# Kernel optimization log

Measured on AMD Instinct MI355X. Metric: run time of the kernel, lower is better.

Reference implementation:

```python
import jax, jax.numpy as jnp
import numpy as np

B, N, C = 4, 4096, 128
IK, CK = 9, 9  # inner_k, cross_k
BN_EPS = 1e-5


def setup_inputs() -> dict:
    key = jax.random.key(0)
    ks = jax.random.split(key, 8)
    d = {}
    d["x"] = jax.random.normal(ks[0], (B, N, C), jnp.float32)
    d["y"] = jax.random.normal(ks[1], (B, N, C), jnp.float32)
    d["x_mask"] = jnp.ones((B, N), jnp.float32)
    d["y_mask"] = jnp.ones((B, N), jnp.float32)
    specs = [("mr0", C, 2 * C), ("mr1", C, 2 * C), ("fc", C, C), ("f1", 4 * C, C), ("f2", C, 4 * C)]
    for (name, o, i), k in zip(specs, jax.random.split(ks[2], len(specs))):
        d[name + "_W"] = jax.random.normal(k, (o, i), jnp.float32) * 0.05
        d[name + "_b"] = jnp.zeros((o,), jnp.float32)
        d[name + "_g"] = jnp.ones((o,), jnp.float32)
        d[name + "_beta"] = jnp.zeros((o,), jnp.float32)
        d[name + "_m"] = jnp.zeros((o,), jnp.float32)
        d[name + "_v"] = jnp.ones((o,), jnp.float32)
    return d


def _sqdist(a, b):
    # a: [B,Na,C], b: [B,Nb,C] -> [B,Na,Nb]
    return (jnp.sum(a * a, -1)[:, :, None] + jnp.sum(b * b, -1)[:, None, :]
            - 2.0 * jnp.einsum('bnc,bmc->bnm', a, b))


def _knn(x, y):
    # neighbor indices into concat([x;y]) for every node: [B, Nx+Ny, IK+CK]
    Nx = x.shape[1]
    i_xx = jax.lax.top_k(-_sqdist(x, x), IK)[1]
    i_xy = jax.lax.top_k(-_sqdist(x, y), CK)[1] + Nx
    i_yy = jax.lax.top_k(-_sqdist(y, y), IK)[1] + Nx
    i_yx = jax.lax.top_k(-_sqdist(y, x), CK)[1]
    return jnp.concatenate([jnp.concatenate([i_xx, i_xy], -1),
                            jnp.concatenate([i_yy, i_yx], -1)], axis=1)


def _bn(h, g, b, m, v):
    # eval-mode BatchNorm over channel (last) axis
    return (h - m) * jax.lax.rsqrt(v + BN_EPS) * g + b


def _gelu(h):
    return jax.nn.gelu(h, approximate=False)


def _mrconv(f, nbr, W, b, g, be, m, v):
    # f: [B,Nt,C], nbr: [B,Nt,K] -> Conv(2C->C)+BN+GELU of interleaved [x, max_j(x_j-x_i)]
    xj = jax.vmap(lambda fb, nb: fb[nb])(f, nbr)          # [B,Nt,K,C] gather
    msg = jnp.max(xj - f[:, :, None, :], axis=2)          # [B,Nt,C]
    Bh, Nt, Ch = f.shape
    h = jnp.stack([f, msg], axis=-1).reshape(Bh, Nt, 2 * Ch)  # channel interleave as in torch reshape
    h = jnp.einsum('bnc,oc->bno', h, W) + b
    return _gelu(_bn(h, g, be, m, v))


def _forward(x, x_mask, y, y_mask,
             mr0_W, mr0_b, mr0_g, mr0_beta, mr0_m, mr0_v,
             mr1_W, mr1_b, mr1_g, mr1_beta, mr1_m, mr1_v,
             fc_W, fc_b, fc_g, fc_beta, fc_m, fc_v,
             f1_W, f1_b, f1_g, f1_beta, f1_m, f1_v,
             f2_W, f2_b, f2_g, f2_beta, f2_m, f2_v):
    Nx = x.shape[1]
    nbr = _knn(x, y)
    xy = jnp.concatenate([x, y], axis=1)
    xy = _mrconv(xy, nbr, mr0_W, mr0_b, mr0_g, mr0_beta, mr0_m, mr0_v) + xy
    xy = _mrconv(xy, nbr, mr1_W, mr1_b, mr1_g, mr1_beta, mr1_m, mr1_v) + xy
    xg, yg = xy[:, :Nx], xy[:, Nx:]

    def fc(h):
        return _bn(jnp.einsum('bnc,oc->bno', h, fc_W) + fc_b, fc_g, fc_beta, fc_m, fc_v)

    xo = fc(xg) + x
    yo = fc(yg) + y

    def ffn(h):
        r = h
        h = _gelu(_bn(jnp.einsum('bnc,oc->bno', h, f1_W) + f1_b, f1_g, f1_beta, f1_m, f1_v))
        h = _gelu(_bn(jnp.einsum('bnc,oc->bno', h, f2_W) + f2_b, f2_g, f2_beta, f2_m, f2_v))
        return h + r

    xo = ffn(xo) * x_mask[:, :, None]
    yo = ffn(yo) * y_mask[:, :, None]
    return xo, yo


def reference(x, x_mask, y, y_mask,
              mr0_W, mr0_b, mr0_g, mr0_beta, mr0_m, mr0_v,
              mr1_W, mr1_b, mr1_g, mr1_beta, mr1_m, mr1_v,
              fc_W, fc_b, fc_g, fc_beta, fc_m, fc_v,
              f1_W, f1_b, f1_g, f1_beta, f1_m, f1_v,
              f2_W, f2_b, f2_g, f2_beta, f2_m, f2_v):
    return _forward(x, x_mask, y, y_mask,
                    mr0_W, mr0_b, mr0_g, mr0_beta, mr0_m, mr0_v,
                    mr1_W, mr1_b, mr1_g, mr1_beta, mr1_m, mr1_v,
                    fc_W, fc_b, fc_g, fc_beta, fc_m, fc_v,
                    f1_W, f1_b, f1_g, f1_beta, f1_m, f1_v,
                    f2_W, f2_b, f2_g, f2_beta, f2_m, f2_v)
```

## Files before the change

### kernel.cpp

```cpp
#include <hip/hip_runtime.h>
#include <hip/hip_bf16.h>
#include <float.h>
#include <math.h>

#define BB 4
#define N1 4096
#define NT 8192
#define CH 128
#define NBRS 18
#define ZSEL 2.35f
#define LCAP 40
#define EQ 4096.0f
#define GQGAP 6
#define GQCOV 3

typedef __attribute__((ext_vector_type(8))) short s16x8;
typedef __attribute__((ext_vector_type(16))) float f32x16;
typedef __attribute__((ext_vector_type(4))) float f32x4;

__device__ inline unsigned short f2bf(float v) {
  unsigned u = __float_as_uint(v);
  unsigned r = (u + 0x7FFFu + ((u >> 16) & 1u)) >> 16;
  return (unsigned short)r;
}
__device__ inline float bf2f(unsigned short h) {
  return __uint_as_float((unsigned)h << 16);
}
__device__ inline unsigned mapf(float f) {
  unsigned u = __float_as_uint(f);
  return (u & 0x80000000u) ? ~u : (u | 0x80000000u);
}
__device__ inline float gelu_f(float x) {
  return 0.5f * x * (1.0f + erff(x * 0.70710678118654752f));
}

__global__ __launch_bounds__(256) void transpose_k(const float* __restrict__ in,
                                                   float* __restrict__ out,
                                                   int rows, int cols) {
  int t = blockIdx.x * 256 + threadIdx.x;
  if (t < rows * cols) {
    int r = t / cols, c = t % cols;
    out[c * rows + r] = in[t];
  }
}

__global__ __launch_bounds__(256) void wsplit_k(const float* __restrict__ w,
                                                unsigned short* __restrict__ hi,
                                                unsigned short* __restrict__ lo,
                                                int n) {
  int t = blockIdx.x * 256 + threadIdx.x;
  if (t < n) {
    float v = w[t];
    unsigned short h = f2bf(v);
    float r = v - bf2f(h);
    hi[t] = h; lo[t] = f2bf(r);
  }
}

__global__ __launch_bounds__(256) void norms_concat_k(const float* __restrict__ x,
                                                      const float* __restrict__ y,
                                                      float* __restrict__ xy,
                                                      float* __restrict__ norms) {
  int w = (blockIdx.x * 256 + threadIdx.x) >> 6;
  int lane = threadIdx.x & 63;
  int b = w >> 13, row = w & 8191;
  const float* src = (row < N1) ? (x + ((size_t)b * N1 + row) * CH)
                                : (y + ((size_t)b * N1 + (row - N1)) * CH);
  float2 v = *(const float2*)(src + lane * 2);
  *(float2*)(xy + (size_t)w * CH + lane * 2) = v;
  float s = v.x * v.x + v.y * v.y;
  for (int off = 32; off > 0; off >>= 1) s += __shfl_down(s, off);
  if (lane == 0) norms[w] = s;
}

__global__ __launch_bounds__(256) void cbt_k(const float* __restrict__ xy,
                                             unsigned short* __restrict__ cbt) {
  int t = blockIdx.x * 256 + threadIdx.x;
  int u = t >> 15, p = t & 32767;
  const float* src = xy + (size_t)p * CH + u * 8;
  unsigned hw[4], lw[4];
#pragma unroll
  for (int j = 0; j < 4; ++j) {
    float v0 = src[2 * j], v1 = src[2 * j + 1];
    unsigned short h0 = f2bf(v0), h1 = f2bf(v1);
    float r0 = v0 - bf2f(h0);
    float r1 = v1 - bf2f(h1);
    unsigned short l0 = f2bf(r0), l1 = f2bf(r1);
    hw[j] = (unsigned)h0 | ((unsigned)h1 << 16);
    lw[j] = (unsigned)l0 | ((unsigned)l1 << 16);
  }
  *(uint4*)&cbt[((size_t)u * 32768 + p) * 8] = make_uint4(hw[0], hw[1], hw[2], hw[3]);
  *(uint4*)&cbt[((size_t)(u + 16) * 32768 + p) * 8] = make_uint4(lw[0], lw[1], lw[2], lw[3]);
}

__global__ __launch_bounds__(256) void knn4_k(const unsigned short* __restrict__ cbt,
                                              const float* __restrict__ norms,
                                              int* __restrict__ nbr,
                                              int* __restrict__ cntg,
                                              unsigned* __restrict__ listA,
                                              unsigned* __restrict__ listB,
                                              unsigned short* __restrict__ fbl) {
  __shared__ unsigned short __align__(16) cst[2][32][32][8];
  __shared__ float cn_s[2][32];
  __shared__ unsigned lst[128][2][LCAP];
  __shared__ unsigned short lcnt[128][2];
  const int tid = threadIdx.x;
  const int qblk = blockIdx.x, z = blockIdx.y;
  const int b = z >> 2, combo = z & 3;
  const int qoff = (combo <= 1) ? 0 : N1;
  const int coff = (combo == 0 || combo == 3) ? 0 : N1;
  const int w = tid >> 6;
  const int cl = tid & 31;
  const int h = (tid >> 5) & 1;
  const int h4 = 4 * h;
  const int ql = w * 32 + cl;
  const int q = qblk * 128 + ql;
  const size_t qp = (size_t)b * NT + qoff + q;
  const size_t cb0 = (size_t)b * NT + coff;

  const s16x8* cv = (const s16x8*)cbt;
  s16x8 bh[8], bl[8];
#pragma unroll
  for (int s = 0; s < 8; ++s) {
    bh[s] = cv[(size_t)(2 * s + h) * 32768 + qp];
    bl[s] = cv[(size_t)(16 + 2 * s + h) * 32768 + qp];
  }

  const float nq = norms[qp];
  const float Tc = 128.f - ZSEL * sqrtf(256.f + 4.f * nq);
  int cnt = 0;

  const int su = tid >> 5, sc = tid & 31;
  const char* p0 = (const char*)&cbt[((size_t)(su) * 32768 + cb0 + sc) * 8];
  const char* p1 = (const char*)&cbt[((size_t)(8 + su) * 32768 + cb0 + sc) * 8];
  const char* p2 = (const char*)&cbt[((size_t)(16 + su) * 32768 + cb0 + sc) * 8];
  const char* p3 = (const char*)&cbt[((size_t)(24 + su) * 32768 + cb0 + sc) * 8];
  const float* pn = norms + cb0 + tid;

  uint4 st[4]; float cnreg = 0.f;
  st[0] = *(const uint4*)p0; p0 += 512;
  st[1] = *(const uint4*)p1; p1 += 512;
  st[2] = *(const uint4*)p2; p2 += 512;
  st[3] = *(const uint4*)p3; p3 += 512;
  if (tid < 32) { cnreg = *pn; pn += 32; }
  *(uint4*)&cst[0][su][sc][0] = st[0];
  *(uint4*)&cst[0][8 + su][sc][0] = st[1];
  *(uint4*)&cst[0][16 + su][sc][0] = st[2];
  *(uint4*)&cst[0][24 + su][sc][0] = st[3];
  if (tid < 32) cn_s[0][tid] = cnreg;
  __syncthreads();

  int buf = 0;
  for (int t = 0; t < 128; ++t) {
    if (t < 127) {
      st[0] = *(const uint4*)p0; p0 += 512;
      st[1] = *(const uint4*)p1; p1 += 512;
      st[2] = *(const uint4*)p2; p2 += 512;
      st[3] = *(const uint4*)p3; p3 += 512;
      if (tid < 32) { cnreg = *pn; pn += 32; }
    }
    f32x16 acc = {0.f,0.f,0.f,0.f,0.f,0.f,0.f,0.f,0.f,0.f,0.f,0.f,0.f,0.f,0.f,0.f};
#pragma unroll
    for (int s = 0; s < 8; ++s) {
      s16x8 a0 = *(const s16x8*)&cst[buf][2 * s + h][cl][0];
      s16x8 a1 = *(const s16x8*)&cst[buf][16 + 2 * s + h][cl][0];
      acc = __builtin_amdgcn_mfma_f32_32x32x16_bf16(a0, bh[s], acc, 0, 0, 0);
      acc = __builtin_amdgcn_mfma_f32_32x32x16_bf16(a0, bl[s], acc, 0, 0, 0);
      acc = __builtin_amdgcn_mfma_f32_32x32x16_bf16(a1, bh[s], acc, 0, 0, 0);
    }
    float4 c0 = *(const float4*)&cn_s[buf][h4];
    float4 c1 = *(const float4*)&cn_s[buf][8 + h4];
    float4 c2 = *(const float4*)&cn_s[buf][16 + h4];
    float4 c3 = *(const float4*)&cn_s[buf][24 + h4];
    const float cw[16] = {c0.x, c0.y, c0.z, c0.w, c1.x, c1.y, c1.z, c1.w,
                          c2.x, c2.y, c2.z, c2.w, c3.x, c3.y, c3.z, c3.w};
    const int ib = t * 32 + h4;
#pragma unroll
    for (int g = 0; g < 4; ++g) {
#pragma unroll
      for (int rr = 0; rr < 4; ++rr) {
        const int r = g * 4 + rr;
        float s = fmaf(-2.0f, acc[r], cw[r]);
        if (s <= Tc) {
          int e = (int)((Tc - s) * EQ);
          e = e > 0xFFFFF ? 0xFFFFF : e;
          unsigned key = ((unsigned)e << 12) | (unsigned)(4095 - (ib + g * 8 + rr));
          if (cnt < LCAP) lst[ql][h][cnt] = key;
          ++cnt;
        }
      }
    }
    if (t < 127) {
      *(uint4*)&cst[buf ^ 1][su][sc][0] = st[0];
      *(uint4*)&cst[buf ^ 1][8 + su][sc][0] = st[1];
      *(uint4*)&cst[buf ^ 1][16 + su][sc][0] = st[2];
      *(uint4*)&cst[buf ^ 1][24 + su][sc][0] = st[3];
      if (tid < 32) cn_s[buf ^ 1][tid] = cnreg;
    }
    __syncthreads();
    buf ^= 1;
  }
  lcnt[ql][h] = (unsigned short)cnt;
  __syncthreads();

  if (tid < 128) {
    const int mq = tid;
    const int gq = z * 4096 + qblk * 128 + mq;
    const int c0 = lcnt[mq][0], c1 = lcnt[mq][1];
    const bool over = (c0 > LCAP) || (c1 > LCAP);
    const int n0 = c0 > LCAP ? LCAP : c0;
    const int n1 = c1 > LCAP ? LCAP : c1;
    const int m = n0 + n1;
    unsigned top[10];
#pragma unroll
    for (int j = 0; j < 10; ++j) top[j] = 0u;
    for (int li = 0; li < 2; ++li) {
      const int n = li ? n1 : n0;
      for (int i = 0; i < n; ++i) {
        unsigned key = lst[mq][li][i];
        if (key > top[9]) {
#pragma unroll
          for (int j = 0; j < 10; ++j) {
            bool sw = key > top[j];
            unsigned tv = top[j];
            top[j] = sw ? key : tv;
            key = sw ? tv : key;
          }
        }
      }
    }
    const unsigned e8 = top[8] >> 12, e9 = top[9] >> 12;
    const bool cov = !over && (m >= 9) && (e8 >= GQCOV);
    const bool ok = cov && (m == 9 || (e8 - e9) >= GQGAP);
    const int qg = qblk * 128 + mq;
    const int row = (combo <= 1) ? qg : (N1 + qg);
    const int slot = (combo == 0 || combo == 2) ? 0 : 9;
    const int ioff = (combo == 1 || combo == 2) ? N1 : 0;
    int* dst = nbr + ((size_t)b * NT + row) * NBRS + slot;
    if (ok) {
#pragma unroll
      for (int s = 0; s < 9; ++s)
        dst[s] = (int)(4095u - (top[s] & 0xFFFu)) + ioff;
    } else if (!cov || m > 64) {
      int idx = atomicAdd(&cntg[1], 1);
      listB[idx] = (unsigned)gq;
    } else {
      int idx = atomicAdd(&cntg[0], 1);
      listA[idx] = ((unsigned)m << 16) | (unsigned)gq;
      unsigned short* fp = fbl + (size_t)gq * 64;
      int p = 0;
      for (int i = 0; i < n0; ++i) fp[p++] = (unsigned short)(4095u - (lst[mq][0][i] & 0xFFFu));
      for (int i = 0; i < n1; ++i) fp[p++] = (unsigned short)(4095u - (lst[mq][1][i] & 0xFFFu));
    }
  }
}

__global__ __launch_bounds__(256) void rerank_sl_k(const float* __restrict__ xy,
                                                   const float* __restrict__ norms,
                                                   const unsigned short* __restrict__ fbl,
                                                   const unsigned* __restrict__ listA,
                                                   const int* __restrict__ cntg,
                                                   int* __restrict__ nbr) {
  const int lane = threadIdx.x & 63;
  const int wv = threadIdx.x >> 6;
  const int nA = cntg[0];
  for (int i = blockIdx.x * 4 + wv; i < nA; i += gridDim.x * 4) {
    const unsigned ent = listA[i];
    const int gq = (int)(ent & 0xffffu);
    const int m = (int)(ent >> 16);
    const int z = gq >> 12, q = gq & 4095;
    const int b = z >> 2, combo = z & 3;
    const int qoff = (combo <= 1) ? 0 : N1;
    const int coff = (combo == 0 || combo == 3) ? 0 : N1;
    const size_t cq = (size_t)b * NT + coff;
    const int row = (combo <= 1) ? q : (N1 + q);
    const int slot = (combo == 0 || combo == 2) ? 0 : 9;
    const int ioff = (combo == 1 || combo == 2) ? N1 : 0;
    int* dst = nbr + ((size_t)b * NT + row) * NBRS + slot;
    const float* qrow = xy + ((size_t)b * NT + qoff + q) * CH;

    int ci = 0; float de = FLT_MAX;
    if (lane < m) {
      ci = (int)fbl[(size_t)gq * 64 + lane];
      const float* crow = xy + (cq + ci) * CH;
      const float cnv = norms[cq + ci];
      float a0 = 0.f, a1 = 0.f, a2 = 0.f, a3 = 0.f;
#pragma unroll
      for (int k = 0; k < 32; ++k) {
        float4 qv = *(const float4*)(qrow + k * 4);
        float4 cv2 = *(const float4*)(crow + k * 4);
        a0 = fmaf(qv.x, cv2.x, a0); a1 = fmaf(qv.y, cv2.y, a1);
        a2 = fmaf(qv.z, cv2.z, a2); a3 = fmaf(qv.w, cv2.w, a3);
      }
      de = cnv - 2.0f * ((a0 + a1) + (a2 + a3));
    }
    unsigned long long key = ((unsigned long long)mapf(de) << 32) | (unsigned)ci;
    if (lane >= m) key = ~0ull;
    int xr = 0;
#pragma unroll 1
    for (int k = 0; k < m; ++k) {
      unsigned long long kk = __shfl(key, k);
      xr += (kk < key) ? 1 : 0;
    }
    if (lane < m && xr < 9) dst[xr] = ci + ioff;
  }
}

__global__ __launch_bounds__(256) void rerank_fs_k(const float* __restrict__ xy,
                                                   const float* __restrict__ norms,
                                                   const unsigned* __restrict__ listB,
                                                   const int* __restrict__ cntg,
                                                   int* __restrict__ nbr) {
  __shared__ unsigned long long ms[4][576];
  __shared__ unsigned long long wk[36];
  const int tid = threadIdx.x;
  const int lane = tid & 63, wv = tid >> 6;
  const int nB = cntg[1];
  for (int i = blockIdx.x; i < nB; i += gridDim.x) {
    const int gq = (int)listB[i];
    const int z = gq >> 12, q = gq & 4095;
    const int b = z >> 2, combo = z & 3;
    const int qoff = (combo <= 1) ? 0 : N1;
    const int coff = (combo == 0 || combo == 3) ? 0 : N1;
    const size_t cq = (size_t)b * NT + coff;
    const int row = (combo <= 1) ? q : (N1 + q);
    const int slot = (combo == 0 || combo == 2) ? 0 : 9;
    const int ioff = (combo == 1 || combo == 2) ? N1 : 0;
    int* dst = nbr + ((size_t)b * NT + row) * NBRS + slot;
    const float* qrow = xy + ((size_t)b * NT + qoff + q) * CH;

    unsigned long long bl9[9];
#pragma unroll
    for (int j = 0; j < 9; ++j) bl9[j] = ~0ull;
    for (int it = 0; it < 16; ++it) {
      const int cc = (it * 4 + wv) * 64 + lane;
      const float* crow = xy + (cq + cc) * CH;
      float a0 = 0.f, a1 = 0.f, a2 = 0.f, a3 = 0.f;
#pragma unroll
      for (int k = 0; k < 32; ++k) {
        float4 qv = *(const float4*)(qrow + k * 4);
        float4 cv2 = *(const float4*)(crow + k * 4);
        a0 = fmaf(qv.x, cv2.x, a0); a1 = fmaf(qv.y, cv2.y, a1);
        a2 = fmaf(qv.z, cv2.z, a2); a3 = fmaf(qv.w, cv2.w, a3);
      }
      float d2v = norms[cq + cc] - 2.0f * ((a0 + a1) + (a2 + a3));
      unsigned long long key = ((unsigned long long)mapf(d2v) << 32) | (unsigned)cc;
      if (key < bl9[8]) {
#pragma unroll
        for (int jj = 0; jj < 9; ++jj) {
          bool sw = key < bl9[jj];
          unsigned long long tv = bl9[jj];
          bl9[jj] = sw ? key : tv;
          key = sw ? tv : key;
        }
      }
    }
#pragma unroll
    for (int s = 0; s < 9; ++s) ms[wv][lane * 9 + s] = bl9[s];
    int ptr = 0;
    for (int s = 0; s < 9; ++s) {
      unsigned long long hd = ms[wv][lane * 9 + ptr];
      unsigned long long mn = hd;
#pragma unroll
      for (int off = 1; off < 64; off <<= 1) {
        unsigned long long ot = __shfl_xor(mn, off);
        mn = (ot < mn) ? ot : mn;
      }
      unsigned long long wm = __ballot(hd == mn);
      int wl = __ffsll(wm) - 1;
      if (lane == wl) ptr++;
      if (lane == 0) wk[wv * 9 + s] = mn;
    }
    __syncthreads();
    if (wv == 0) {
      unsigned long long key = (lane < 36) ? wk[lane] : ~0ull;
      int xr = 0;
#pragma unroll 1
      for (int k = 0; k < 36; ++k) {
        unsigned long long kk = __shfl(key, k);
        xr += (kk < key) ? 1 : 0;
      }
      if (lane < 36 && xr < 9) dst[xr] = (int)(unsigned)(key & 0xffffffffull) + ioff;
    }
    __syncthreads();
  }
}

__global__ __launch_bounds__(256) void mrconv_k(const float* __restrict__ in,
                                                const int* __restrict__ nbr,
                                                const float* __restrict__ Wt,
                                                const float* __restrict__ bias,
                                                const float* __restrict__ gam,
                                                const float* __restrict__ bet,
                                                const float* __restrict__ mean,
                                                const float* __restrict__ var,
                                                float* __restrict__ out) {
  __shared__ float h[32][260];
  const int tid = threadIdx.x;
  const int pt0 = blockIdx.x * 32;
  {
    const int w = tid >> 6, lane = tid & 63;
    for (int pp = 0; pp < 8; ++pp) {
      const int p = w * 8 + pp;
      const int n = pt0 + p;
      const int b = n >> 13;
      const float* frow = in + (size_t)n * CH;
      float2 f2 = *(const float2*)(frow + lane * 2);
      float mx = -FLT_MAX, my = -FLT_MAX;
      const int* nb = nbr + (size_t)n * NBRS;
      for (int j = 0; j < NBRS; ++j) {
        int idx = nb[j];
        const float* vrow = in + ((size_t)b * NT + idx) * CH;
        float2 v2 = *(const float2*)(vrow + lane * 2);
        mx = fmaxf(mx, v2.x - f2.x);
        my = fmaxf(my, v2.y - f2.y);
      }
      h[p][lane * 4 + 0] = f2.x; h[p][lane * 4 + 1] = mx;
      h[p][lane * 4 + 2] = f2.y; h[p][lane * 4 + 3] = my;
    }
  }
  __syncthreads();
  const int o = tid & 127, gg = tid >> 7;
  float acc[16];
#pragma unroll
  for (int p = 0; p < 16; ++p) acc[p] = 0.f;
  for (int k = 0; k < 256; k += 4) {
    float w0 = Wt[(k + 0) * CH + o], w1 = Wt[(k + 1) * CH + o];
    float w2 = Wt[(k + 2) * CH + o], w3 = Wt[(k + 3) * CH + o];
#pragma unroll
    for (int p = 0; p < 16; ++p) {
      float4 hv = *(const float4*)&h[gg * 16 + p][k];
      acc[p] = fmaf(hv.x, w0, acc[p]);
      acc[p] = fmaf(hv.y, w1, acc[p]);
      acc[p] = fmaf(hv.z, w2, acc[p]);
      acc[p] = fmaf(hv.w, w3, acc[p]);
    }
  }
  const float sc = gam[o] / sqrtf(var[o] + 1e-5f);
  const float bs = bias[o], mo = mean[o], be = bet[o];
#pragma unroll
  for (int p = 0; p < 16; ++p) {
    const int n = pt0 + gg * 16 + p;
    float hv = acc[p] + bs;
    float bn = (hv - mo) * sc + be;
    float gl = 0.5f * bn * (1.0f + erff(bn * 0.70710678118654752f));
    out[(size_t)n * CH + o] = gl + h[gg * 16 + p][2 * o];
  }
}

__global__ __launch_bounds__(256) void fc2_k(const float* __restrict__ in,
                                             const unsigned short* __restrict__ Whi,
                                             const unsigned short* __restrict__ Wlo,
                                             const float* __restrict__ bias,
                                             const float* __restrict__ gam,
                                             const float* __restrict__ bet,
                                             const float* __restrict__ mean,
                                             const float* __restrict__ var,
                                             const float* __restrict__ xres,
                                             const float* __restrict__ yres,
                                             float* __restrict__ out) {
  __shared__ unsigned short __align__(16) aHi[16][16][8];
  __shared__ unsigned short __align__(16) aLo[16][16][8];
  const int tid = threadIdx.x;
  const int pt0 = blockIdx.x * 16;
  {
    const int row = tid >> 4, ku = tid & 15;
    const float* src = in + (size_t)(pt0 + row) * CH + ku * 8;
    unsigned hw[4], lw[4];
#pragma unroll
    for (int j = 0; j < 4; ++j) {
      float v0 = src[2 * j], v1 = src[2 * j + 1];
      unsigned short h0 = f2bf(v0), h1 = f2bf(v1);
      float r0 = v0 - bf2f(h0), r1 = v1 - bf2f(h1);
      hw[j] = (unsigned)h0 | ((unsigned)f2bf(v1) << 16);
      hw[j] = (unsigned)h0 | ((unsigned)h1 << 16);
      lw[j] = (unsigned)f2bf(r0) | ((unsigned)f2bf(r1) << 16);
    }
    *(uint4*)&aHi[ku][row][0] = make_uint4(hw[0], hw[1], hw[2], hw[3]);
    *(uint4*)&aLo[ku][row][0] = make_uint4(lw[0], lw[1], lw[2], lw[3]);
  }
  __syncthreads();
  const int lane = tid & 63, w = tid >> 6;
  const int r16 = lane & 15, kg = lane >> 4;
  f32x4 acc[2] = {{0.f,0.f,0.f,0.f}, {0.f,0.f,0.f,0.f}};
#pragma unroll
  for (int ks = 0; ks < 4; ++ks) {
    s16x8 ah = *(const s16x8*)&aHi[ks * 4 + kg][r16][0];
    s16x8 al = *(const s16x8*)&aLo[ks * 4 + kg][r16][0];
#pragma unroll
    for (int cb = 0; cb < 2; ++cb) {
      const int o = w * 32 + cb * 16 + r16;
      s16x8 bh2 = *(const s16x8*)(Whi + o * 128 + ks * 32 + kg * 8);
      s16x8 bl2 = *(const s16x8*)(Wlo + o * 128 + ks * 32 + kg * 8);
      acc[cb] = __builtin_amdgcn_mfma_f32_16x16x32_bf16(ah, bh2, acc[cb], 0, 0, 0);
      acc[cb] = __builtin_amdgcn_mfma_f32_16x16x32_bf16(ah, bl2, acc[cb], 0, 0, 0);
      acc[cb] = __builtin_amdgcn_mfma_f32_16x16x32_bf16(al, bh2, acc[cb], 0, 0, 0);
    }
  }
#pragma unroll
  for (int cb = 0; cb < 2; ++cb) {
    const int o = w * 32 + cb * 16 + r16;
    const float sc = gam[o] / sqrtf(var[o] + 1e-5f);
    const float bs = bias[o], mo = mean[o], be = bet[o];
#pragma unroll
    for (int rg = 0; rg < 4; ++rg) {
      const int row = kg * 4 + rg;
      const int n = pt0 + row;
      const int b = n >> 13, prow = n & 8191;
      float bn = (acc[cb][rg] + bs - mo) * sc + be;
      float res = (prow < N1) ? xres[((size_t)b * N1 + prow) * CH + o]
                              : yres[((size_t)b * N1 + prow - N1) * CH + o];
      out[(size_t)n * CH + o] = bn + res;
    }
  }
}

__global__ __launch_bounds__(256) void ffn2_k(const float* __restrict__ u,
                                              const unsigned short* __restrict__ W1hi,
                                              const unsigned short* __restrict__ W1lo,
                                              const float* __restrict__ b1,
                                              const float* __restrict__ g1,
                                              const float* __restrict__ be1,
                                              const float* __restrict__ m1,
                                              const float* __restrict__ v1,
                                              const unsigned short* __restrict__ W2hi,
                                              const unsigned short* __restrict__ W2lo,
                                              const float* __restrict__ b2,
                                              const float* __restrict__ g2,
                                              const float* __restrict__ be2,
                                              const float* __restrict__ m2,
                                              const float* __restrict__ v2,
                                              const float* __restrict__ xmask,
                                              const float* __restrict__ ymask,
                                              float* __restrict__ outbuf) {
  __shared__ unsigned short __align__(16) aHi[16][16][8];
  __shared__ unsigned short __align__(16) aLo[16][16][8];
  __shared__ unsigned short __align__(16) hHi[64][16][8];
  __shared__ unsigned short __align__(16) hLo[64][16][8];
  const int tid = threadIdx.x;
  const int pt0 = blockIdx.x * 16;
  {
    const int row = tid >> 4, ku = tid & 15;
    const float* src = u + (size_t)(pt0 + row) * CH + ku * 8;
    unsigned hw[4], lw[4];
#pragma unroll
    for (int j = 0; j < 4; ++j) {
      float v0 = src[2 * j], v1 = src[2 * j + 1];
      unsigned short h0 = f2bf(v0), h1 = f2bf(v1);
      float r0 = v0 - bf2f(h0), r1 = v1 - bf2f(h1);
      hw[j] = (unsigned)h0 | ((unsigned)h1 << 16);
      lw[j] = (unsigned)f2bf(r0) | ((unsigned)f2bf(r1) << 16);
    }
    *(uint4*)&aHi[ku][row][0] = make_uint4(hw[0], hw[1], hw[2], hw[3]);
    *(uint4*)&aLo[ku][row][0] = make_uint4(lw[0], lw[1], lw[2], lw[3]);
  }
  __syncthreads();
  const int lane = tid & 63, w = tid >> 6;
  const int r16 = lane & 15, kg = lane >> 4;
  {
    f32x4 acc[8];
#pragma unroll
    for (int cb = 0; cb < 8; ++cb) acc[cb] = {0.f, 0.f, 0.f, 0.f};
#pragma unroll
    for (int ks = 0; ks < 4; ++ks) {
      s16x8 ah = *(const s16x8*)&aHi[ks * 4 + kg][r16][0];
      s16x8 al = *(const s16x8*)&aLo[ks * 4 + kg][r16][0];
#pragma unroll
      for (int cb = 0; cb < 8; ++cb) {
        const int o = w * 128 + cb * 16 + r16;
        s16x8 bh2 = *(const s16x8*)(W1hi + o * 128 + ks * 32 + kg * 8);
        s16x8 bl2 = *(const s16x8*)(W1lo + o * 128 + ks * 32 + kg * 8);
        acc[cb] = __builtin_amdgcn_mfma_f32_16x16x32_bf16(ah, bh2, acc[cb], 0, 0, 0);
        acc[cb] = __builtin_amdgcn_mfma_f32_16x16x32_bf16(ah, bl2, acc[cb], 0, 0, 0);
        acc[cb] = __builtin_amdgcn_mfma_f32_16x16x32_bf16(al, bh2, acc[cb], 0, 0, 0);
      }
    }
#pragma unroll
    for (int cb = 0; cb < 8; ++cb) {
      const int o = w * 128 + cb * 16 + r16;
      const float sc = g1[o] / sqrtf(v1[o] + 1e-5f);
      const float bs = b1[o], mo = m1[o], be = be1[o];
#pragma unroll
      for (int rg = 0; rg < 4; ++rg) {
        const int row = kg * 4 + rg;
        float bn = (acc[cb][rg] + bs - mo) * sc + be;
        float gl = gelu_f(bn);
        unsigned short hb = f2bf(gl);
        float rr = gl - bf2f(hb);
        hHi[o >> 3][row][o & 7] = hb;
        hLo[o >> 3][row][o & 7] = f2bf(rr);
      }
    }
  }
  __syncthreads();
  {
    f32x4 acc[2] = {{0.f,0.f,0.f,0.f}, {0.f,0.f,0.f,0.f}};
#pragma unroll
    for (int ks = 0; ks < 16; ++ks) {
      s16x8 ah = *(const s16x8*)&hHi[ks * 4 + kg][r16][0];
      s16x8 al = *(const s16x8*)&hLo[ks * 4 + kg][r16][0];
#pragma unroll
      for (int cb = 0; cb < 2; ++cb) {
        const int o = w * 32 + cb * 16 + r16;
        s16x8 bh2 = *(const s16x8*)(W2hi + o * 512 + ks * 32 + kg * 8);
        s16x8 bl2 = *(const s16x8*)(W2lo + o * 512 + ks * 32 + kg * 8);
        acc[cb] = __builtin_amdgcn_mfma_f32_16x16x32_bf16(ah, bh2, acc[cb], 0, 0, 0);
        acc[cb] = __builtin_amdgcn_mfma_f32_16x16x32_bf16(ah, bl2, acc[cb], 0, 0, 0);
        acc[cb] = __builtin_amdgcn_mfma_f32_16x16x32_bf16(al, bh2, acc[cb], 0, 0, 0);
      }
    }
#pragma unroll
    for (int cb = 0; cb < 2; ++cb) {
      const int o = w * 32 + cb * 16 + r16;
      const float sc = g2[o] / sqrtf(v2[o] + 1e-5f);
      const float bs = b2[o], mo = m2[o], be = be2[o];
#pragma unroll
      for (int rg = 0; rg < 4; ++rg) {
        const int row = kg * 4 + rg;
        const int n = pt0 + row;
        const int b = n >> 13, prow = n & 8191;
        float bn = (acc[cb][rg] + bs - mo) * sc + be;
        float gl = gelu_f(bn);
        float res = u[(size_t)n * CH + o];
        float msk; size_t oidx;
        if (prow < N1) {
          msk = xmask[(size_t)b * N1 + prow];
          oidx = ((size_t)b * N1 + prow) * CH + o;
        } else {
          msk = ymask[(size_t)b * N1 + prow - N1];
          oidx = (size_t)BB * N1 * CH + ((size_t)b * N1 + prow - N1) * CH + o;
        }
        outbuf[oidx] = (gl + res) * msk;
      }
    }
  }
}

extern "C" void kernel_launch(void* const* d_in, const int* in_sizes, int n_in,
                              void* d_out, int out_size, void* d_ws, size_t ws_size,
                              hipStream_t stream) {
  const float* x  = (const float*)d_in[0];
  const float* y  = (const float*)d_in[1];
  const float* xm = (const float*)d_in[2];
  const float* ym = (const float*)d_in[3];
  const float* mr0W = (const float*)d_in[4];
  const float* mr1W = (const float*)d_in[10];
  const float* fcW  = (const float*)d_in[16];
  const float* f1W  = (const float*)d_in[22];
  const float* f2W  = (const float*)d_in[28];

  char* ws = (char*)d_ws;
  float*          xyA   = (float*)(ws + 0);
  unsigned short* cbt   = (unsigned short*)(ws + 16777216);
  float*          xyB   = (float*)(ws + 16777216);
  float*          norms = (float*)(ws + 33554432);
  int*            cntg  = (int*)(ws + 33685504);
  unsigned*       listA = (unsigned*)(ws + 33689600);
  unsigned*       listB = (unsigned*)(ws + 33951744);
  unsigned short* fbl   = (unsigned short*)(ws + 34213888);
  int*            nbr   = (int*)(ws + 42602496);
  float*          mr0t  = (float*)(ws + 44961792);
  float*          mr1t  = (float*)(ws + 45092864);
  unsigned short* fcWhi = (unsigned short*)(ws + 45223936);
  unsigned short* fcWlo = (unsigned short*)(ws + 45256704);
  unsigned short* f1hi  = (unsigned short*)(ws + 45289472);
  unsigned short* f1lo  = (unsigned short*)(ws + 45420544);
  unsigned short* f2hi  = (unsigned short*)(ws + 45551616);
  unsigned short* f2lo  = (unsigned short*)(ws + 45682688);

  hipMemsetAsync(cntg, 0, 8, stream);

  transpose_k<<<(128 * 256 + 255) / 256, 256, 0, stream>>>(mr0W, mr0t, 128, 256);
  transpose_k<<<(128 * 256 + 255) / 256, 256, 0, stream>>>(mr1W, mr1t, 128, 256);
  wsplit_k<<<64, 256, 0, stream>>>(fcW, fcWhi, fcWlo, 128 * 128);
  wsplit_k<<<256, 256, 0, stream>>>(f1W, f1hi, f1lo, 512 * 128);
  wsplit_k<<<256, 256, 0, stream>>>(f2W, f2hi, f2lo, 128 * 512);

  norms_concat_k<<<8192, 256, 0, stream>>>(x, y, xyA, norms);
  cbt_k<<<2048, 256, 0, stream>>>(xyA, cbt);
  knn4_k<<<dim3(32, 16), 256, 0, stream>>>(cbt, norms, nbr, cntg, listA, listB, fbl);
  rerank_sl_k<<<256, 256, 0, stream>>>(xyA, norms, fbl, listA, cntg, nbr);
  rerank_fs_k<<<256, 256, 0, stream>>>(xyA, norms, listB, cntg, nbr);

  mrconv_k<<<1024, 256, 0, stream>>>(xyA, nbr, mr0t,
      (const float*)d_in[5], (const float*)d_in[6], (const float*)d_in[7],
      (const float*)d_in[8], (const float*)d_in[9], xyB);
  mrconv_k<<<1024, 256, 0, stream>>>(xyB, nbr, mr1t,
      (const float*)d_in[11], (const float*)d_in[12], (const float*)d_in[13],
      (const float*)d_in[14], (const float*)d_in[15], xyA);

  fc2_k<<<2048, 256, 0, stream>>>(xyA, fcWhi, fcWlo,
      (const float*)d_in[17], (const float*)d_in[18], (const float*)d_in[19],
      (const float*)d_in[20], (const float*)d_in[21], x, y, xyB);

  ffn2_k<<<2048, 256, 0, stream>>>(xyB,
      f1hi, f1lo, (const float*)d_in[23], (const float*)d_in[24], (const float*)d_in[25],
      (const float*)d_in[26], (const float*)d_in[27],
      f2hi, f2lo, (const float*)d_in[29], (const float*)d_in[30], (const float*)d_in[31],
      (const float*)d_in[32], (const float*)d_in[33],
      xm, ym, (float*)d_out);
}
```

Measured before the change: 623.0 us.

## Use split-bf16 MFMA for MRConv projection instead of scalar FP32 FMA

The MRConv 2C->C projection now runs on bf16 MFMA instructions, with the activations and weights split into hi/lo bf16 parts and three MFMAs per tile to keep near-fp32 accuracy. The weight transpose kernels are replaced by wsplit kernels that produce the hi/lo bf16 weights in row-major layout. This removes the scalar FMA loop and its per-k global weight loads. In exchange it converts the activations from shared memory on every k-step, which adds ALU work.

Result: faster. 576.1 us, median of 2 (-7.5%).

```diff
diff --git a/kernel.cpp b/kernel.cpp
--- a/kernel.cpp
+++ b/kernel.cpp
@@ -32,16 +32,6 @@
 }
 __device__ inline float gelu_f(float x) {
   return 0.5f * x * (1.0f + erff(x * 0.70710678118654752f));
-}
-
-__global__ __launch_bounds__(256) void transpose_k(const float* __restrict__ in,
-                                                   float* __restrict__ out,
-                                                   int rows, int cols) {
-  int t = blockIdx.x * 256 + threadIdx.x;
-  if (t < rows * cols) {
-    int r = t / cols, c = t % cols;
-    out[c * rows + r] = in[t];
-  }
 }
 
 __global__ __launch_bounds__(256) void wsplit_k(const float* __restrict__ w,
@@ -386,15 +376,16 @@
   }
 }
 
-__global__ __launch_bounds__(256) void mrconv_k(const float* __restrict__ in,
-                                                const int* __restrict__ nbr,
-                                                const float* __restrict__ Wt,
-                                                const float* __restrict__ bias,
-                                                const float* __restrict__ gam,
-                                                const float* __restrict__ bet,
-                                                const float* __restrict__ mean,
-                                                const float* __restrict__ var,
-                                                float* __restrict__ out) {
+__global__ __launch_bounds__(256) void mrconv2_k(const float* __restrict__ in,
+                                                 const int* __restrict__ nbr,
+                                                 const unsigned short* __restrict__ Whi,
+                                                 const unsigned short* __restrict__ Wlo,
+                                                 const float* __restrict__ bias,
+                                                 const float* __restrict__ gam,
+                                                 const float* __restrict__ bet,
+                                                 const float* __restrict__ mean,
+                                                 const float* __restrict__ var,
+                                                 float* __restrict__ out) {
   __shared__ float h[32][260];
   const int tid = threadIdx.x;
   const int pt0 = blockIdx.x * 32;
@@ -420,31 +411,54 @@
     }
   }
   __syncthreads();
-  const int o = tid & 127, gg = tid >> 7;
-  float acc[16];
-#pragma unroll
-  for (int p = 0; p < 16; ++p) acc[p] = 0.f;
-  for (int k = 0; k < 256; k += 4) {
-    float w0 = Wt[(k + 0) * CH + o], w1 = Wt[(k + 1) * CH + o];
-    float w2 = Wt[(k + 2) * CH + o], w3 = Wt[(k + 3) * CH + o];
-#pragma unroll
-    for (int p = 0; p < 16; ++p) {
-      float4 hv = *(const float4*)&h[gg * 16 + p][k];
-      acc[p] = fmaf(hv.x, w0, acc[p]);
-      acc[p] = fmaf(hv.y, w1, acc[p]);
-      acc[p] = fmaf(hv.z, w2, acc[p]);
-      acc[p] = fmaf(hv.w, w3, acc[p]);
-    }
-  }
-  const float sc = gam[o] / sqrtf(var[o] + 1e-5f);
-  const float bs = bias[o], mo = mean[o], be = bet[o];
-#pragma unroll
-  for (int p = 0; p < 16; ++p) {
-    const int n = pt0 + gg * 16 + p;
-    float hv = acc[p] + bs;
-    float bn = (hv - mo) * sc + be;
-    float gl = 0.5f * bn * (1.0f + erff(bn * 0.70710678118654752f));
-    out[(size_t)n * CH + o] = gl + h[gg * 16 + p][2 * o];
+  const int lane = tid & 63, w = tid >> 6;
+  const int r16 = lane & 15, kg = lane >> 4;
+  f32x4 acc[2][2] = {{{0.f,0.f,0.f,0.f},{0.f,0.f,0.f,0.f}},
+                     {{0.f,0.f,0.f,0.f},{0.f,0.f,0.f,0.f}}};
+#pragma unroll
+  for (int ks = 0; ks < 8; ++ks) {
+    s16x8 ah[2], al[2];
+#pragma unroll
+    for (int rt = 0; rt < 2; ++rt) {
+      const float* hp = &h[rt * 16 + r16][(ks * 4 + kg) * 8];
+#pragma unroll
+      for (int j = 0; j < 8; ++j) {
+        float v = hp[j];
+        unsigned short hb = f2bf(v);
+        float rr = v - bf2f(hb);
+        ah[rt][j] = (short)hb;
+        al[rt][j] = (short)f2bf(rr);
+      }
+    }
+#pragma unroll
+    for (int cbi = 0; cbi < 2; ++cbi) {
+      const int o = (w * 2 + cbi) * 16 + r16;
+      s16x8 bh2 = *(const s16x8*)(Whi + o * 256 + ks * 32 + kg * 8);
+      s16x8 bl2 = *(const s16x8*)(Wlo + o * 256 + ks * 32 + kg * 8);
+#pragma unroll
+      for (int rt = 0; rt < 2; ++rt) {
+        acc[rt][cbi] = __builtin_amdgcn_mfma_f32_16x16x32_bf16(ah[rt], bh2, acc[rt][cbi], 0, 0, 0);
+        acc[rt][cbi] = __builtin_amdgcn_mfma_f32_16x16x32_bf16(ah[rt], bl2, acc[rt][cbi], 0, 0, 0);
+        acc[rt][cbi] = __builtin_amdgcn_mfma_f32_16x16x32_bf16(al[rt], bh2, acc[rt][cbi], 0, 0, 0);
+      }
+    }
+  }
+#pragma unroll
+  for (int cbi = 0; cbi < 2; ++cbi) {
+    const int o = (w * 2 + cbi) * 16 + r16;
+    const float sc = gam[o] / sqrtf(var[o] + 1e-5f);
+    const float bs = bias[o], mo = mean[o], be = bet[o];
+#pragma unroll
+    for (int rt = 0; rt < 2; ++rt) {
+#pragma unroll
+      for (int rg = 0; rg < 4; ++rg) {
+        const int row = rt * 16 + kg * 4 + rg;
+        const int n = pt0 + row;
+        float bn = (acc[rt][cbi][rg] + bs - mo) * sc + be;
+        float gl = gelu_f(bn);
+        out[(size_t)n * CH + o] = gl + h[row][2 * o];
+      }
+    }
   }
 }
 
@@ -472,7 +486,6 @@
       float v0 = src[2 * j], v1 = src[2 * j + 1];
       unsigned short h0 = f2bf(v0), h1 = f2bf(v1);
       float r0 = v0 - bf2f(h0), r1 = v1 - bf2f(h1);
-      hw[j] = (unsigned)h0 | ((unsigned)f2bf(v1) << 16);
       hw[j] = (unsigned)h0 | ((unsigned)h1 << 16);
       lw[j] = (unsigned)f2bf(r0) | ((unsigned)f2bf(r1) << 16);
     }
@@ -659,8 +672,10 @@
   unsigned*       listB = (unsigned*)(ws + 33951744);
   unsigned short* fbl   = (unsigned short*)(ws + 34213888);
   int*            nbr   = (int*)(ws + 42602496);
-  float*          mr0t  = (float*)(ws + 44961792);
-  float*          mr1t  = (float*)(ws + 45092864);
+  unsigned short* mr0hi = (unsigned short*)(ws + 44961792);
+  unsigned short* mr0lo = (unsigned short*)(ws + 45027328);
+  unsigned short* mr1hi = (unsigned short*)(ws + 45092864);
+  unsigned short* mr1lo = (unsigned short*)(ws + 45158400);
   unsigned short* fcWhi = (unsigned short*)(ws + 45223936);
   unsigned short* fcWlo = (unsigned short*)(ws + 45256704);
   unsigned short* f1hi  = (unsigned short*)(ws + 45289472);
@@ -670,8 +685,8 @@
 
   hipMemsetAsync(cntg, 0, 8, stream);
 
-  transpose_k<<<(128 * 256 + 255) / 256, 256, 0, stream>>>(mr0W, mr0t, 128, 256);
-  transpose_k<<<(128 * 256 + 255) / 256, 256, 0, stream>>>(mr1W, mr1t, 128, 256);
+  wsplit_k<<<128, 256, 0, stream>>>(mr0W, mr0hi, mr0lo, 128 * 256);
+  wsplit_k<<<128, 256, 0, stream>>>(mr1W, mr1hi, mr1lo, 128 * 256);
   wsplit_k<<<64, 256, 0, stream>>>(fcW, fcWhi, fcWlo, 128 * 128);
   wsplit_k<<<256, 256, 0, stream>>>(f1W, f1hi, f1lo, 512 * 128);
   wsplit_k<<<256, 256, 0, stream>>>(f2W, f2hi, f2lo, 128 * 512);
@@ -682,10 +697,10 @@
   rerank_sl_k<<<256, 256, 0, stream>>>(xyA, norms, fbl, listA, cntg, nbr);
   rerank_fs_k<<<256, 256, 0, stream>>>(xyA, norms, listB, cntg, nbr);
 
-  mrconv_k<<<1024, 256, 0, stream>>>(xyA, nbr, mr0t,
+  mrconv2_k<<<1024, 256, 0, stream>>>(xyA, nbr, mr0hi, mr0lo,
       (const float*)d_in[5], (const float*)d_in[6], (const float*)d_in[7],
       (const float*)d_in[8], (const float*)d_in[9], xyB);
-  mrconv_k<<<1024, 256, 0, stream>>>(xyB, nbr, mr1t,
+  mrconv2_k<<<1024, 256, 0, stream>>>(xyB, nbr, mr1hi, mr1lo,
       (const float*)d_in[11], (const float*)d_in[12], (const float*)d_in[13],
       (const float*)d_in[14], (const float*)d_in[15], xyA);
 
```
